# Kernel tuning notes

Hardware: AMD Instinct MI355X
Metric: run time of the kernel (lower is better)

## Reference

```python
import jax, jax.numpy as jnp
import numpy as np

NHEAD = 12
EPS = 1e-5


def layernorm_nobias(x, gamma):
    mu = jnp.mean(x, axis=-1, keepdims=True)
    var = jnp.var(x, axis=-1, keepdims=True)
    return (x - mu) * jax.lax.rsqrt(var + EPS) * gamma


def setup_inputs() -> dict:
    key = jax.random.key(0)
    ks = jax.random.split(key, 10)
    b, l, d = 4, 2048, 768
    s = d ** -0.5
    return {
        "x": jax.random.normal(ks[0], (b, l, d), jnp.float32),
        "Wq": jax.random.normal(ks[1], (d, d), jnp.float32) * s,
        "Wk": jax.random.normal(ks[2], (d, d), jnp.float32) * s,
        "bk": jax.random.normal(ks[3], (d,), jnp.float32) * 0.02,
        "Wv": jax.random.normal(ks[4], (d, d), jnp.float32) * s,
        "bv": jax.random.normal(ks[5], (d,), jnp.float32) * 0.02,
        "gq": jnp.ones((d,), jnp.float32),
        "gk": jnp.ones((d,), jnp.float32),
        "Wo": jax.random.normal(ks[6], (d, d), jnp.float32) * s,
        "bo": jnp.zeros((d,), jnp.float32),
    }


def reference(x, Wq, Wk, bk, Wv, bv, gq, gk, Wo, bo):
    b, l, d = x.shape
    n = NHEAD
    hd = d // n
    scale = hd ** -0.5
    # projections (torch Linear: x @ W.T + b), QK-norm over full dmodel
    q = layernorm_nobias(x @ Wq.T, gq)
    k = layernorm_nobias(x @ Wk.T + bk, gk)
    v = x @ Wv.T + bv
    # split heads: b l (n hd) -> b n l hd
    q = q.reshape(b, l, n, hd).transpose(0, 2, 1, 3)
    k = k.reshape(b, l, n, hd).transpose(0, 2, 1, 3)
    v = v.reshape(b, l, n, hd).transpose(0, 2, 1, 3)
    # scores [b, n, l_q, l_k]; NOTE: softmax over the QUERY axis (dim=-2)
    scores = jnp.einsum('bnqd,bnkd->bnqk', q, k) * scale
    attn = jax.nn.softmax(scores, axis=-2)
    o = jnp.einsum('bnqk,bnkd->bnqd', attn, v)
    o = o.transpose(0, 2, 1, 3).reshape(b, l, d)
    return o @ Wo.T + bo + x
```

## Files before the change

kernel.cpp:

```cpp
#include <hip/hip_runtime.h>
#include <cstddef>
#include <cstdint>


typedef unsigned short u16;
typedef short  bf16x8 __attribute__((ext_vector_type(8)));
typedef float  f32x4  __attribute__((ext_vector_type(4)));
typedef unsigned short u16x8 __attribute__((ext_vector_type(8)));
typedef unsigned short u16x4 __attribute__((ext_vector_type(4)));

#define B_   4
#define L_   2048
#define D_   768
#define NH_  12
#define HD_  64
#define M_   (B_*L_)
#define SC2  (0.125f * 1.44269504088896f)

__device__ __forceinline__ float ex2(float x) { return __builtin_amdgcn_exp2f(x); }

__device__ __forceinline__ u16 f2bf(float f) {
    union { float f; unsigned u; } v; v.f = f;
    unsigned r = v.u + 0x7FFFu + ((v.u >> 16) & 1u);
    return (u16)(r >> 16);
}
__device__ __forceinline__ float bf2f(u16 b) {
    union { unsigned u; float f; } v; v.u = ((unsigned)b) << 16;
    return v.f;
}
__device__ __forceinline__ unsigned fbits(float f) {
    union { float f; unsigned u; } v; v.f = f; return v.u;
}
__device__ __forceinline__ unsigned packbf(float lo, float hi) {
    return __builtin_amdgcn_perm(fbits(hi), fbits(lo), 0x07060302u);
}

__device__ __forceinline__ void gld16(const void* g, void* l) {
    __builtin_amdgcn_global_load_lds(
        (const __attribute__((address_space(1))) unsigned*)g,
        (__attribute__((address_space(3))) unsigned*)l, 16, 0, 0);
}

__global__ __launch_bounds__(256) void cvt_all(
    const float* __restrict__ X,
    const float* __restrict__ W0, const float* __restrict__ W1,
    const float* __restrict__ W2, const float* __restrict__ W3,
    u16* __restrict__ Yx,
    u16* __restrict__ Y0, u16* __restrict__ Y1,
    u16* __restrict__ Y2, u16* __restrict__ Y3)
{
    const int nX8 = (M_ * D_) / 8;
    const int nW8 = (D_ * D_) / 8;
    int i = blockIdx.x * 256 + threadIdx.x;
    if (i >= nX8 + 4 * nW8) return;
    const float* S; u16* Dst; int off;
    if (i < nX8) { S = X; Dst = Yx; off = i; }
    else {
        int j = i - nX8;
        int w = j / nW8; off = j - w * nW8;
        S   = (w == 0) ? W0 : (w == 1) ? W1 : (w == 2) ? W2 : W3;
        Dst = (w == 0) ? Y0 : (w == 1) ? Y1 : (w == 2) ? Y2 : Y3;
    }
    const float4* xp = (const float4*)S + (size_t)off * 2;
    float4 a = xp[0], b = xp[1];
    u16x8 o;
    o[0] = f2bf(a.x); o[1] = f2bf(a.y); o[2] = f2bf(a.z); o[3] = f2bf(a.w);
    o[4] = f2bf(b.x); o[5] = f2bf(b.y); o[6] = f2bf(b.z); o[7] = f2bf(b.w);
    *((u16x8*)Dst + off) = o;
}

__global__ __launch_bounds__(256, 4) void gemm_qkv(
    const u16* __restrict__ A,
    const u16* __restrict__ W0, const u16* __restrict__ W1,
    const u16* __restrict__ W2,
    const float* __restrict__ bk, const float* __restrict__ bv,
    u16* __restrict__ q_o, u16* __restrict__ k_o, u16* __restrict__ v_o)
{
    __shared__ __align__(16) u16 lds[16384];
    __shared__ float bs[128];
    const int tid  = threadIdx.x;
    const int lane = tid & 63, w = tid >> 6;
    const int s    = lane & 15, quad = lane >> 4;
    const int bid  = blockIdx.x;
    const int xcd  = bid & 7, j0 = bid >> 3;
    const int bm   = (xcd * 8 + j0 / 18) * 128;
    const int sub  = j0 % 18;
    const int seg  = sub / 6;
    const int bn   = (sub % 6) * 128;
    const u16* W = (seg == 0) ? W0 : ((seg == 1) ? W1 : W2);
    u16* OUT = (seg == 0) ? q_o : ((seg == 1) ? k_o : v_o);
    const int mh = (w >> 1) * 64, nh = (w & 1) * 64;
    const int wb = tid & ~63;
    const int cq = quad ^ ((s >> 1) & 3);

    if (tid < 128)
        bs[tid] = (seg == 1) ? bk[bn + tid] : ((seg == 2) ? bv[bn + tid] : 0.0f);

    f32x4 acc[4][4];
    #pragma unroll
    for (int j = 0; j < 4; ++j)
        #pragma unroll
        for (int i = 0; i < 4; ++i) acc[j][i] = (f32x4){0.f, 0.f, 0.f, 0.f};

    {
        int c = tid, r = c >> 2, cs = (c & 3) ^ ((r >> 1) & 3);
        gld16(A + (size_t)(bm + r) * D_ + cs * 8, lds + (size_t)wb * 8);
        gld16(W + (size_t)(bn + r) * D_ + cs * 8, lds + 8192 + (size_t)wb * 8);
        c = tid + 256; r = c >> 2; cs = (c & 3) ^ ((r >> 1) & 3);
        gld16(A + (size_t)(bm + r) * D_ + cs * 8, lds + (size_t)(wb + 256) * 8);
        gld16(W + (size_t)(bn + r) * D_ + cs * 8, lds + 8192 + (size_t)(wb + 256) * 8);
    }
    __syncthreads();

    for (int t = 0; t < 24; ++t) {
        const u16* Ab = lds + (t & 1) * 4096;
        const u16* Bb = lds + 8192 + (t & 1) * 4096;
        if (t < 23) {
            const int k0 = (t + 1) * 32;
            u16* Ad = lds + ((t + 1) & 1) * 4096;
            u16* Bd = lds + 8192 + ((t + 1) & 1) * 4096;
            int c = tid, r = c >> 2, cs = (c & 3) ^ ((r >> 1) & 3);
            gld16(A + (size_t)(bm + r) * D_ + k0 + cs * 8, Ad + (size_t)wb * 8);
            gld16(W + (size_t)(bn + r) * D_ + k0 + cs * 8, Bd + (size_t)wb * 8);
            c = tid + 256; r = c >> 2; cs = (c & 3) ^ ((r >> 1) & 3);
            gld16(A + (size_t)(bm + r) * D_ + k0 + cs * 8, Ad + (size_t)(wb + 256) * 8);
            gld16(W + (size_t)(bn + r) * D_ + k0 + cs * 8, Bd + (size_t)(wb + 256) * 8);
        }
        bf16x8 af[4], bf[4];
        #pragma unroll
        for (int i = 0; i < 4; ++i)
            af[i] = *(const bf16x8*)(Ab + (mh + i * 16 + s) * 32 + cq * 8);
        #pragma unroll
        for (int j = 0; j < 4; ++j)
            bf[j] = *(const bf16x8*)(Bb + (nh + j * 16 + s) * 32 + cq * 8);
        #pragma unroll
        for (int j = 0; j < 4; ++j)
            #pragma unroll
            for (int i = 0; i < 4; ++i)
                acc[j][i] = __builtin_amdgcn_mfma_f32_16x16x32_bf16(
                    bf[j], af[i], acc[j][i], 0, 0, 0);
        __syncthreads();
    }
    u16* Ct = lds;
    #pragma unroll
    for (int j = 0; j < 4; ++j) {
        const int n0 = nh + j * 16 + quad * 4;
        const f32x4 b4 = *(const f32x4*)(bs + n0);
        const int cn = n0 >> 3, off = n0 & 7;
        #pragma unroll
        for (int i = 0; i < 4; ++i) {
            const int m = mh + i * 16 + s;
            u16x4 ov;
            #pragma unroll
            for (int r = 0; r < 4; ++r) ov[r] = f2bf(acc[j][i][r] + b4[r]);
            *(u16x4*)(Ct + m * 128 + ((cn ^ (m & 15)) * 8) + off) = ov;
        }
    }
    __syncthreads();
    {
        const int m = tid >> 1, half = tid & 1;
        u16* dst = OUT + (size_t)(bm + m) * D_ + bn + half * 64;
        #pragma unroll
        for (int cc = 0; cc < 8; ++cc) {
            const int cn = half * 8 + cc;
            u16x8 v = *(const u16x8*)(Ct + m * 128 + ((cn ^ (m & 15)) * 8));
            *(u16x8*)(dst + cc * 8) = v;
        }
    }
}

__global__ __launch_bounds__(256, 3) void gemm_final(
    const u16* __restrict__ A, const u16* __restrict__ W,
    const float* __restrict__ bias, const float* __restrict__ resid,
    float* __restrict__ outf)
{
    __shared__ __align__(16) u16 lds[16384];
    const int tid  = threadIdx.x;
    const int lane = tid & 63, w = tid >> 6;
    const int s    = lane & 15, quad = lane >> 4;
    const int bid  = blockIdx.x;
    const int xcd  = bid & 7, j0 = bid >> 3;
    const int bm   = (xcd * 8 + j0 / 6) * 128;
    const int bn   = (j0 % 6) * 128;
    const int mh   = (w >> 1) * 64, nh = (w & 1) * 64;
    const int wb   = tid & ~63;
    const int cq   = quad ^ ((s >> 1) & 3);
    f32x4 acc[4][4];
    #pragma unroll
    for (int j = 0; j < 4; ++j)
        #pragma unroll
        for (int i = 0; i < 4; ++i) acc[j][i] = (f32x4){0.f, 0.f, 0.f, 0.f};

    {
        int c = tid, r = c >> 2, cs = (c & 3) ^ ((r >> 1) & 3);
        gld16(A + (size_t)(bm + r) * D_ + cs * 8, lds + (size_t)wb * 8);
        gld16(W + (size_t)(bn + r) * D_ + cs * 8, lds + 8192 + (size_t)wb * 8);
        c = tid + 256; r = c >> 2; cs = (c & 3) ^ ((r >> 1) & 3);
        gld16(A + (size_t)(bm + r) * D_ + cs * 8, lds + (size_t)(wb + 256) * 8);
        gld16(W + (size_t)(bn + r) * D_ + cs * 8, lds + 8192 + (size_t)(wb + 256) * 8);
    }
    __syncthreads();

    for (int t = 0; t < 24; ++t) {
        const u16* Ab = lds + (t & 1) * 4096;
        const u16* Bb = lds + 8192 + (t & 1) * 4096;
        if (t < 23) {
            const int k0 = (t + 1) * 32;
            u16* Ad = lds + ((t + 1) & 1) * 4096;
            u16* Bd = lds + 8192 + ((t + 1) & 1) * 4096;
            int c = tid, r = c >> 2, cs = (c & 3) ^ ((r >> 1) & 3);
            gld16(A + (size_t)(bm + r) * D_ + k0 + cs * 8, Ad + (size_t)wb * 8);
            gld16(W + (size_t)(bn + r) * D_ + k0 + cs * 8, Bd + (size_t)wb * 8);
            c = tid + 256; r = c >> 2; cs = (c & 3) ^ ((r >> 1) & 3);
            gld16(A + (size_t)(bm + r) * D_ + k0 + cs * 8, Ad + (size_t)(wb + 256) * 8);
            gld16(W + (size_t)(bn + r) * D_ + k0 + cs * 8, Bd + (size_t)(wb + 256) * 8);
        }
        bf16x8 af[4], bf[4];
        #pragma unroll
        for (int i = 0; i < 4; ++i)
            af[i] = *(const bf16x8*)(Ab + (mh + i * 16 + s) * 32 + cq * 8);
        #pragma unroll
        for (int j = 0; j < 4; ++j)
            bf[j] = *(const bf16x8*)(Bb + (nh + j * 16 + s) * 32 + cq * 8);
        #pragma unroll
        for (int j = 0; j < 4; ++j)
            #pragma unroll
            for (int i = 0; i < 4; ++i)
                acc[j][i] = __builtin_amdgcn_mfma_f32_16x16x32_bf16(
                    bf[j], af[i], acc[j][i], 0, 0, 0);
        __syncthreads();
    }
    #pragma unroll
    for (int j = 0; j < 4; ++j) {
        const int n0 = nh + j * 16 + quad * 4;
        const float4 b4 = *(const float4*)(bias + bn + n0);
        #pragma unroll
        for (int i = 0; i < 4; ++i) {
            const int m = mh + i * 16 + s;
            const size_t base = (size_t)(bm + m) * D_ + bn + n0;
            const float4 rs = *(const float4*)(resid + base);
            float4 o;
            o.x = acc[j][i][0] + b4.x + rs.x;
            o.y = acc[j][i][1] + b4.y + rs.y;
            o.z = acc[j][i][2] + b4.z + rs.z;
            o.w = acc[j][i][3] + b4.w + rs.w;
            *(float4*)(outf + base) = o;
        }
    }
}

__global__ __launch_bounds__(256) void ln2_bf16(
    const u16* __restrict__ Q, const u16* __restrict__ K,
    const float* __restrict__ gq, const float* __restrict__ gk,
    u16* __restrict__ Yq, u16* __restrict__ Yk)
{
    const int row = blockIdx.x;
    const int which = blockIdx.y;
    const u16* x = (which ? K : Q) + (size_t)row * D_;
    const float* gamma = which ? gk : gq;
    u16* Y = which ? Yk : Yq;
    const float scale = which ? 1.0f : (float)SC2;
    const int tid = threadIdx.x;
    float v[3];
    float lsum = 0.f, lsq = 0.f;
    #pragma unroll
    for (int e = 0; e < 3; ++e) {
        float t = bf2f(x[tid + e * 256]);
        v[e] = t; lsum += t; lsq += t * t;
    }
    #pragma unroll
    for (int off = 32; off > 0; off >>= 1) {
        lsum += __shfl_down(lsum, off);
        lsq  += __shfl_down(lsq,  off);
    }
    __shared__ float s1[4], s2[4];
    const int wv = tid >> 6, lane = tid & 63;
    if (lane == 0) { s1[wv] = lsum; s2[wv] = lsq; }
    __syncthreads();
    const float sum = s1[0] + s1[1] + s1[2] + s1[3];
    const float sq  = s2[0] + s2[1] + s2[2] + s2[3];
    const float mu  = sum * (1.0f / D_);
    const float var = sq * (1.0f / D_) - mu * mu;
    const float inv = rsqrtf(var + 1e-5f) * scale;
    #pragma unroll
    for (int e = 0; e < 3; ++e) {
        int c = tid + e * 256;
        Y[(size_t)row * D_ + c] = f2bf((v[e] - mu) * inv * gamma[c]);
    }
}

__global__ __launch_bounds__(256, 3) void attn_stats(
    const u16* __restrict__ Qb, const u16* __restrict__ Kb,
    float* __restrict__ Rl)
{
    __shared__ __align__(16) u16 Ks[128 * 64];
    __shared__ __align__(16) u16 Qs[2][128 * 64];
    __shared__ float lbuf[4][64];
    const int tid  = threadIdx.x;
    const int lane = tid & 63, w = tid >> 6;
    const int s    = lane & 15, quad = lane >> 4;
    const int s7   = s & 7;
    const int bid  = blockIdx.x;
    const int xcd  = bid & 7, j0 = bid >> 3;
    const int bh   = xcd * 6 + j0 / 16;
    const int kbase = (j0 % 16) * 128;
    const int b    = bh / NH_, h = bh % NH_;
    const u16* Qg = Qb + (size_t)b * L_ * D_ + h * HD_;
    const u16* Kg = Kb + (size_t)b * L_ * D_ + h * HD_;
    const int mh = (w >> 1) * 64;
    const int nh = (w & 1) * 64;
    const int wb = tid & ~63;

    #pragma unroll
    for (int c0 = 0; c0 < 1024; c0 += 256) {
        int c = c0 + tid, r = c >> 3, cc = (c & 7) ^ (r & 7);
        gld16(Kg + (size_t)(kbase + r) * D_ + cc * 8, Ks + (size_t)(c0 + wb) * 8);
        gld16(Qg + (size_t)r * D_ + cc * 8, Qs[0] + (size_t)(c0 + wb) * 8);
    }
    __syncthreads();
    bf16x8 kf[2][4];
    #pragma unroll
    for (int kk = 0; kk < 2; ++kk)
        #pragma unroll
        for (int i = 0; i < 4; ++i)
            kf[kk][i] = *(const bf16x8*)(Ks + (mh + i * 16 + s) * 64 +
                                         ((kk * 4 + quad) ^ s7) * 8);
    float lacc[4][4];
    #pragma unroll
    for (int i = 0; i < 4; ++i)
        #pragma unroll
        for (int r = 0; r < 4; ++r) lacc[i][r] = 0.f;

    for (int t = 0; t < 16; ++t) {
        if (t < 15) {
            const int qn = (t + 1) * 128;
            u16* Qd = Qs[(t + 1) & 1];
            #pragma unroll
            for (int c0 = 0; c0 < 1024; c0 += 256) {
                int c = c0 + tid, r = c >> 3, cc = (c & 7) ^ (r & 7);
                gld16(Qg + (size_t)(qn + r) * D_ + cc * 8, Qd + (size_t)(c0 + wb) * 8);
            }
        }
        const u16* Qt = Qs[t & 1];
        f32x4 acc[4][4];
        #pragma unroll
        for (int i = 0; i < 4; ++i)
            #pragma unroll
            for (int j = 0; j < 4; ++j) acc[i][j] = (f32x4){0.f, 0.f, 0.f, 0.f};
        #pragma unroll
        for (int kk = 0; kk < 2; ++kk) {
            bf16x8 bf[4];
            #pragma unroll
            for (int j = 0; j < 4; ++j)
                bf[j] = *(const bf16x8*)(Qt + (nh + j * 16 + s) * 64 +
                                         ((kk * 4 + quad) ^ s7) * 8);
            __builtin_amdgcn_s_setprio(1);
            #pragma unroll
            for (int i = 0; i < 4; ++i)
                #pragma unroll
                for (int j = 0; j < 4; ++j)
                    acc[i][j] = __builtin_amdgcn_mfma_f32_16x16x32_bf16(
                        kf[kk][i], bf[j], acc[i][j], 0, 0, 0);
            __builtin_amdgcn_s_setprio(0);
        }
        #pragma unroll
        for (int i = 0; i < 4; ++i)
            #pragma unroll
            for (int r = 0; r < 4; ++r) {
                float l0 = ex2(acc[i][0][r]) + ex2(acc[i][1][r]);
                float l1 = ex2(acc[i][2][r]) + ex2(acc[i][3][r]);
                lacc[i][r] += l0 + l1;
            }
        __syncthreads();
    }
    #pragma unroll
    for (int i = 0; i < 4; ++i)
        #pragma unroll
        for (int r = 0; r < 4; ++r) {
            float v = lacc[i][r];
            #pragma unroll
            for (int d2 = 1; d2 < 16; d2 <<= 1) v += __shfl_xor(v, d2);
            lacc[i][r] = v;
        }
    if (s == 0) {
        #pragma unroll
        for (int i = 0; i < 4; ++i)
            #pragma unroll
            for (int r = 0; r < 4; ++r)
                lbuf[w][i * 16 + quad * 4 + r] = lacc[i][r];
    }
    __syncthreads();
    if (tid < 128) {
        int kh = tid >> 6, kl = tid & 63;
        float l = lbuf[kh * 2][kl] + lbuf[kh * 2 + 1][kl];
        Rl[(size_t)bh * L_ + kbase + tid] = 1.0f / l;
    }
}

__global__ __launch_bounds__(256) void transpose_v_scaled(
    const u16* __restrict__ Vb, const float* __restrict__ Rl,
    u16* __restrict__ Vt)
{
    const int l0 = blockIdx.x * 64, h = blockIdx.y, b = blockIdx.z;
    const int bh = b * NH_ + h;
    __shared__ __align__(16) u16 Ts[64][72];
    const int tid = threadIdx.x;
    #pragma unroll
    for (int c = tid; c < 512; c += 256) {
        int r = c >> 3, cc = c & 7;
        u16x8 val = *(const u16x8*)(Vb + (size_t)(b * L_ + l0 + r) * D_ + h * HD_ + cc * 8);
        const float rl = Rl[(size_t)bh * L_ + l0 + r];
        #pragma unroll
        for (int e = 0; e < 8; ++e) val[e] = f2bf(bf2f(val[e]) * rl);
        *(u16x8*)(&Ts[r][cc * 8]) = val;
    }
    __syncthreads();
    const int d = tid >> 2, lc = (tid & 3) * 16;
    u16 tmp[16];
    #pragma unroll
    for (int e = 0; e < 16; ++e) tmp[e] = Ts[lc + e][d];
    u16* dst = Vt + ((size_t)bh * HD_ + d) * L_ + l0 + (lc & 32) + ((lc >> 4) & 1) * 4;
    #pragma unroll
    for (int qd = 0; qd < 4; ++qd) {
        u16x4 o;
        #pragma unroll
        for (int e = 0; e < 4; ++e) o[e] = tmp[qd * 4 + e];
        *(u16x4*)(dst + qd * 8) = o;
    }
}

__global__ __launch_bounds__(256, 3) void attn_out(
    const u16* __restrict__ Qb, const u16* __restrict__ Kb,
    const u16* __restrict__ Vt, u16* __restrict__ Ob)
{
    __shared__ __align__(16) u16 Ks[3][64 * 64];
    __shared__ __align__(16) u16 Vts[3][64 * 64];
    const int tid  = threadIdx.x;
    const int lane = tid & 63, w = tid >> 6;
    const int s    = lane & 15, quad = lane >> 4;
    const int s7   = s & 7;
    const int bid  = blockIdx.x;
    const int xcd  = bid & 7, j0 = bid >> 3;
    const int bh   = xcd * 6 + j0 / 16;
    const int qbase = (j0 % 16) * 128;
    const int b    = bh / NH_, h = bh % NH_;
    const int qw   = w * 32;
    const u16* Qg = Qb + (size_t)b * L_ * D_ + h * HD_;
    const u16* Kg = Kb + (size_t)b * L_ * D_ + h * HD_;
    const u16* Vg = Vt + (size_t)bh * HD_ * L_;
    const int wb = tid & ~63;

    bf16x8 qf[2][2];
    #pragma unroll
    for (int kk = 0; kk < 2; ++kk)
        #pragma unroll
        for (int j = 0; j < 2; ++j)
            qf[kk][j] = *(const bf16x8*)(
                Qg + (size_t)(qbase + qw + j * 16 + s) * D_ + (kk * 4 + quad) * 8);

    #pragma unroll
    for (int t0 = 0; t0 < 2; ++t0) {
        const int kn = t0 * 64;
        u16* Kd = Ks[t0];
        u16* Vd = Vts[t0];
        int c = tid, r = c >> 3, cc = (c & 7) ^ (r & 7);
        gld16(Kg + (size_t)(kn + r) * D_ + cc * 8, Kd + (size_t)wb * 8);
        gld16(Vg + (size_t)r * L_ + kn + cc * 8,   Vd + (size_t)wb * 8);
        c = tid + 256; r = c >> 3; cc = (c & 7) ^ (r & 7);
        gld16(Kg + (size_t)(kn + r) * D_ + cc * 8, Kd + (size_t)(wb + 256) * 8);
        gld16(Vg + (size_t)r * L_ + kn + cc * 8,   Vd + (size_t)(wb + 256) * 8);
    }
    __syncthreads();

    f32x4 acc_o[4][2];
    #pragma unroll
    for (int i = 0; i < 4; ++i)
        #pragma unroll
        for (int j = 0; j < 2; ++j) acc_o[i][j] = (f32x4){0.f, 0.f, 0.f, 0.f};

    for (int t = 0; t < 32; ++t) {
        const int bi = t % 3;
        const u16* Kt  = Ks[bi];
        const u16* Vtt = Vts[bi];
        if (t + 2 < 32) {
            const int pi = (t + 2) % 3;
            const int kn = (t + 2) * 64;
            u16* Kd = Ks[pi];
            u16* Vd = Vts[pi];
            int c = tid, r = c >> 3, cc = (c & 7) ^ (r & 7);
            gld16(Kg + (size_t)(kn + r) * D_ + cc * 8, Kd + (size_t)wb * 8);
            gld16(Vg + (size_t)r * L_ + kn + cc * 8,   Vd + (size_t)(wb) * 8);
            c = tid + 256; r = c >> 3; cc = (c & 7) ^ (r & 7);
            gld16(Kg + (size_t)(kn + r) * D_ + cc * 8, Kd + (size_t)(wb + 256) * 8);
            gld16(Vg + (size_t)r * L_ + kn + cc * 8,   Vd + (size_t)(wb + 256) * 8);
        }
        f32x4 acc_s[4][2];
        #pragma unroll
        for (int i = 0; i < 4; ++i)
            #pragma unroll
            for (int j = 0; j < 2; ++j) acc_s[i][j] = (f32x4){0.f, 0.f, 0.f, 0.f};
        #pragma unroll
        for (int kk = 0; kk < 2; ++kk) {
            bf16x8 kfr[4];
            #pragma unroll
            for (int i = 0; i < 4; ++i)
                kfr[i] = *(const bf16x8*)(Kt + (i * 16 + s) * 64 +
                                          ((kk * 4 + quad) ^ s7) * 8);
            __builtin_amdgcn_s_setprio(1);
            #pragma unroll
            for (int i = 0; i < 4; ++i)
                #pragma unroll
                for (int j = 0; j < 2; ++j)
                    acc_s[i][j] = __builtin_amdgcn_mfma_f32_16x16x32_bf16(
                        kfr[i], qf[kk][j], acc_s[i][j], 0, 0, 0);
            __builtin_amdgcn_s_setprio(0);
        }
        unsigned pk[4][2][2];
        #pragma unroll
        for (int i = 0; i < 4; ++i)
            #pragma unroll
            for (int j = 0; j < 2; ++j) {
                float p0 = ex2(acc_s[i][j][0]), p1 = ex2(acc_s[i][j][1]);
                float p2 = ex2(acc_s[i][j][2]), p3 = ex2(acc_s[i][j][3]);
                pk[i][j][0] = packbf(p0, p1);
                pk[i][j][1] = packbf(p2, p3);
            }
        #pragma unroll
        for (int kk = 0; kk < 2; ++kk) {
            bf16x8 av[4];
            #pragma unroll
            for (int i = 0; i < 4; ++i)
                av[i] = *(const bf16x8*)(Vtt + (i * 16 + s) * 64 +
                                         ((kk * 4 + quad) ^ s7) * 8);
            __builtin_amdgcn_s_setprio(1);
            #pragma unroll
            for (int j = 0; j < 2; ++j) {
                union { unsigned u[4]; bf16x8 v; } bu;
                bu.u[0] = pk[2 * kk][j][0];
                bu.u[1] = pk[2 * kk][j][1];
                bu.u[2] = pk[2 * kk + 1][j][0];
                bu.u[3] = pk[2 * kk + 1][j][1];
                #pragma unroll
                for (int i = 0; i < 4; ++i)
                    acc_o[i][j] = __builtin_amdgcn_mfma_f32_16x16x32_bf16(
                        av[i], bu.v, acc_o[i][j], 0, 0, 0);
            }
            __builtin_amdgcn_s_setprio(0);
        }
        if (t < 30) {
            asm volatile("s_waitcnt vmcnt(4)" ::: "memory");
            __builtin_amdgcn_s_barrier();
        } else if (t == 30) {
            asm volatile("s_waitcnt vmcnt(0)" ::: "memory");
            __builtin_amdgcn_s_barrier();
        }
    }
    __syncthreads();
    u16* Ep = (u16*)Ks;
    #pragma unroll
    for (int i = 0; i < 4; ++i) {
        const int dchunk = i * 2 + (quad >> 1), doff = (quad & 1) * 4;
        #pragma unroll
        for (int j = 0; j < 2; ++j) {
            const int q = qw + j * 16 + s;
            u16x4 ov;
            #pragma unroll
            for (int r = 0; r < 4; ++r) ov[r] = f2bf(acc_o[i][j][r]);
            *(u16x4*)(Ep + q * 64 + (dchunk ^ s7) * 8 + doff) = ov;
        }
    }
    __syncthreads();
    {
        const int q = tid >> 1, half = tid & 1, q7 = q & 7;
        u16* dst = Ob + (size_t)(b * L_ + qbase + q) * D_ + h * HD_ + half * 32;
        #pragma unroll
        for (int c = 0; c < 4; ++c) {
            const int cn = half * 4 + c;
            u16x8 v = *(const u16x8*)(Ep + q * 64 + ((cn ^ q7) * 8));
            *(u16x8*)(dst + c * 8) = v;
        }
    }
}

extern "C" void kernel_launch(void* const* d_in, const int* in_sizes, int n_in,
                              void* d_out, int out_size, void* d_ws, size_t ws_size,
                              hipStream_t stream)
{
    const float* x  = (const float*)d_in[0];
    const float* Wq = (const float*)d_in[1];
    const float* Wk = (const float*)d_in[2];
    const float* bk = (const float*)d_in[3];
    const float* Wv = (const float*)d_in[4];
    const float* bv = (const float*)d_in[5];
    const float* gq = (const float*)d_in[6];
    const float* gk = (const float*)d_in[7];
    const float* Wo = (const float*)d_in[8];
    const float* bo = (const float*)d_in[9];
    float* out = (float*)d_out;

    char* p = (char*)d_ws;
    u16* xb   = (u16*)p;  p += (size_t)M_ * D_ * 2;
    u16* qpre = (u16*)p;  p += (size_t)M_ * D_ * 2;
    u16* kpre = (u16*)p;  p += (size_t)M_ * D_ * 2;
    u16* vb   = (u16*)p;  p += (size_t)M_ * D_ * 2;
    u16* qb   = (u16*)p;  p += (size_t)M_ * D_ * 2;
    u16* kb   = (u16*)p;  p += (size_t)M_ * D_ * 2;
    u16* wqb  = (u16*)p;  p += (size_t)D_ * D_ * 2;
    u16* wkb  = (u16*)p;  p += (size_t)D_ * D_ * 2;
    u16* wvb  = (u16*)p;  p += (size_t)D_ * D_ * 2;
    u16* wob  = (u16*)p;  p += (size_t)D_ * D_ * 2;
    float* Rl = (float*)p; p += (size_t)B_ * NH_ * L_ * 4;
    u16* ob = qpre;
    u16* vt = kpre;

    const int nTot8 = (M_ * D_ + 4 * D_ * D_) / 8;
    cvt_all<<<(nTot8 + 255) / 256, 256, 0, stream>>>(
        x, Wq, Wk, Wv, Wo, xb, wqb, wkb, wvb, wob);

    gemm_qkv<<<1152, 256, 0, stream>>>(
        xb, wqb, wkb, wvb, bk, bv, qpre, kpre, vb);

    ln2_bf16<<<dim3(M_, 2), 256, 0, stream>>>(qpre, kpre, gq, gk, qb, kb);

    attn_stats<<<768, 256, 0, stream>>>(qb, kb, Rl);
    transpose_v_scaled<<<dim3(L_ / 64, NH_, B_), 256, 0, stream>>>(vb, Rl, vt);
    attn_out<<<768, 256, 0, stream>>>(qb, kb, vt, ob);

    gemm_final<<<384, 256, 0, stream>>>(ob, wob, bo, x, out);
}
```

Baseline: 273.6 us.

## Software-pipeline attention loop so next tile's QK^T overlaps current tile's PV

Restructures the attention inner loop into a two-stage software pipeline. The scores for tile t+1 are computed with MFMA while tile t's exp2 and PV MFMAs run, using two ping-pong score accumulators. The loop is unrolled by two via a macro. The prologue is also reordered to issue K loads before V loads and to wait only for K(0..1) and V0 (vmcnt(2)) rather than a full sync, so the first QK^T starts earlier. The aim is to hide the exp/pack latency and the dependency stall between QK^T and PV, at the cost of more accumulator registers, which may reduce occupancy. The priority boost on the QK MFMAs is dropped.

```diff
diff --git a/kernel.cpp b/kernel.cpp
--- a/kernel.cpp
+++ b/kernel.cpp
@@ -458,19 +458,20 @@
             qf[kk][j] = *(const bf16x8*)(
                 Qg + (size_t)(qbase + qw + j * 16 + s) * D_ + (kk * 4 + quad) * 8);
 
-    #pragma unroll
-    for (int t0 = 0; t0 < 2; ++t0) {
-        const int kn = t0 * 64;
-        u16* Kd = Ks[t0];
-        u16* Vd = Vts[t0];
+    {
         int c = tid, r = c >> 3, cc = (c & 7) ^ (r & 7);
-        gld16(Kg + (size_t)(kn + r) * D_ + cc * 8, Kd + (size_t)wb * 8);
-        gld16(Vg + (size_t)r * L_ + kn + cc * 8,   Vd + (size_t)wb * 8);
-        c = tid + 256; r = c >> 3; cc = (c & 7) ^ (r & 7);
-        gld16(Kg + (size_t)(kn + r) * D_ + cc * 8, Kd + (size_t)(wb + 256) * 8);
-        gld16(Vg + (size_t)r * L_ + kn + cc * 8,   Vd + (size_t)(wb + 256) * 8);
-    }
-    __syncthreads();
+        int c2 = tid + 256, r2 = c2 >> 3, cc2 = (c2 & 7) ^ (r2 & 7);
+        gld16(Kg + (size_t)r * D_ + cc * 8,          Ks[0] + (size_t)wb * 8);
+        gld16(Kg + (size_t)r2 * D_ + cc2 * 8,        Ks[0] + (size_t)(wb + 256) * 8);
+        gld16(Kg + (size_t)(64 + r) * D_ + cc * 8,   Ks[1] + (size_t)wb * 8);
+        gld16(Kg + (size_t)(64 + r2) * D_ + cc2 * 8, Ks[1] + (size_t)(wb + 256) * 8);
+        gld16(Vg + (size_t)r * L_ + cc * 8,          Vts[0] + (size_t)wb * 8);
+        gld16(Vg + (size_t)r2 * L_ + cc2 * 8,        Vts[0] + (size_t)(wb + 256) * 8);
+        gld16(Vg + (size_t)r * L_ + 64 + cc * 8,     Vts[1] + (size_t)wb * 8);
+        gld16(Vg + (size_t)r2 * L_ + 64 + cc2 * 8,   Vts[1] + (size_t)(wb + 256) * 8);
+    }
+    asm volatile("s_waitcnt vmcnt(2)" ::: "memory");
+    __builtin_amdgcn_s_barrier();
 
     f32x4 acc_o[4][2];
     #pragma unroll
@@ -478,83 +479,120 @@
         #pragma unroll
         for (int j = 0; j < 2; ++j) acc_o[i][j] = (f32x4){0.f, 0.f, 0.f, 0.f};
 
-    for (int t = 0; t < 32; ++t) {
-        const int bi = t % 3;
-        const u16* Kt  = Ks[bi];
-        const u16* Vtt = Vts[bi];
-        if (t + 2 < 32) {
-            const int pi = (t + 2) % 3;
-            const int kn = (t + 2) * 64;
-            u16* Kd = Ks[pi];
-            u16* Vd = Vts[pi];
-            int c = tid, r = c >> 3, cc = (c & 7) ^ (r & 7);
-            gld16(Kg + (size_t)(kn + r) * D_ + cc * 8, Kd + (size_t)wb * 8);
-            gld16(Vg + (size_t)r * L_ + kn + cc * 8,   Vd + (size_t)(wb) * 8);
-            c = tid + 256; r = c >> 3; cc = (c & 7) ^ (r & 7);
-            gld16(Kg + (size_t)(kn + r) * D_ + cc * 8, Kd + (size_t)(wb + 256) * 8);
-            gld16(Vg + (size_t)r * L_ + kn + cc * 8,   Vd + (size_t)(wb + 256) * 8);
-        }
-        f32x4 acc_s[4][2];
-        #pragma unroll
-        for (int i = 0; i < 4; ++i)
-            #pragma unroll
-            for (int j = 0; j < 2; ++j) acc_s[i][j] = (f32x4){0.f, 0.f, 0.f, 0.f};
-        #pragma unroll
-        for (int kk = 0; kk < 2; ++kk) {
-            bf16x8 kfr[4];
-            #pragma unroll
-            for (int i = 0; i < 4; ++i)
-                kfr[i] = *(const bf16x8*)(Kt + (i * 16 + s) * 64 +
-                                          ((kk * 4 + quad) ^ s7) * 8);
-            __builtin_amdgcn_s_setprio(1);
-            #pragma unroll
-            for (int i = 0; i < 4; ++i)
-                #pragma unroll
-                for (int j = 0; j < 2; ++j)
-                    acc_s[i][j] = __builtin_amdgcn_mfma_f32_16x16x32_bf16(
-                        kfr[i], qf[kk][j], acc_s[i][j], 0, 0, 0);
-            __builtin_amdgcn_s_setprio(0);
-        }
-        unsigned pk[4][2][2];
-        #pragma unroll
-        for (int i = 0; i < 4; ++i)
-            #pragma unroll
-            for (int j = 0; j < 2; ++j) {
-                float p0 = ex2(acc_s[i][j][0]), p1 = ex2(acc_s[i][j][1]);
-                float p2 = ex2(acc_s[i][j][2]), p3 = ex2(acc_s[i][j][3]);
-                pk[i][j][0] = packbf(p0, p1);
-                pk[i][j][1] = packbf(p2, p3);
-            }
-        #pragma unroll
-        for (int kk = 0; kk < 2; ++kk) {
-            bf16x8 av[4];
-            #pragma unroll
-            for (int i = 0; i < 4; ++i)
-                av[i] = *(const bf16x8*)(Vtt + (i * 16 + s) * 64 +
-                                         ((kk * 4 + quad) ^ s7) * 8);
-            __builtin_amdgcn_s_setprio(1);
-            #pragma unroll
-            for (int j = 0; j < 2; ++j) {
-                union { unsigned u[4]; bf16x8 v; } bu;
-                bu.u[0] = pk[2 * kk][j][0];
-                bu.u[1] = pk[2 * kk][j][1];
-                bu.u[2] = pk[2 * kk + 1][j][0];
-                bu.u[3] = pk[2 * kk + 1][j][1];
-                #pragma unroll
-                for (int i = 0; i < 4; ++i)
-                    acc_o[i][j] = __builtin_amdgcn_mfma_f32_16x16x32_bf16(
-                        av[i], bu.v, acc_o[i][j], 0, 0, 0);
-            }
-            __builtin_amdgcn_s_setprio(0);
-        }
-        if (t < 30) {
-            asm volatile("s_waitcnt vmcnt(4)" ::: "memory");
-            __builtin_amdgcn_s_barrier();
-        } else if (t == 30) {
-            asm volatile("s_waitcnt vmcnt(0)" ::: "memory");
-            __builtin_amdgcn_s_barrier();
-        }
-    }
+    f32x4 acc_s0[4][2], acc_s1[4][2];
+    #pragma unroll
+    for (int i = 0; i < 4; ++i)
+        #pragma unroll
+        for (int j = 0; j < 2; ++j) acc_s0[i][j] = (f32x4){0.f, 0.f, 0.f, 0.f};
+    #pragma unroll
+    for (int kk = 0; kk < 2; ++kk) {
+        bf16x8 kfr[4];
+        #pragma unroll
+        for (int i = 0; i < 4; ++i)
+            kfr[i] = *(const bf16x8*)(Ks[0] + (i * 16 + s) * 64 +
+                                      ((kk * 4 + quad) ^ s7) * 8);
+        #pragma unroll
+        for (int i = 0; i < 4; ++i)
+            #pragma unroll
+            for (int j = 0; j < 2; ++j)
+                acc_s0[i][j] = __builtin_amdgcn_mfma_f32_16x16x32_bf16(
+                    kfr[i], qf[kk][j], acc_s0[i][j], 0, 0, 0);
+    }
+
+#define ATTN_TILE(ACCC, ACCN, TT, DO_PF, DO_S, WMODE)                          \
+    do {                                                                       \
+        const int t_ = (TT);                                                   \
+        if (DO_PF) {                                                           \
+            const int pi_ = (t_ + 2) % 3;                                      \
+            const int kn_ = (t_ + 2) * 64;                                     \
+            u16* Kd_ = Ks[pi_]; u16* Vd_ = Vts[pi_];                           \
+            int c_ = tid, r_ = c_ >> 3, cc_ = (c_ & 7) ^ (r_ & 7);             \
+            int c2_ = tid + 256, r2_ = c2_ >> 3, cc2_ = (c2_ & 7) ^ (r2_ & 7); \
+            gld16(Kg + (size_t)(kn_ + r_) * D_ + cc_ * 8,                      \
+                  Kd_ + (size_t)wb * 8);                                       \
+            gld16(Kg + (size_t)(kn_ + r2_) * D_ + cc2_ * 8,                    \
+                  Kd_ + (size_t)(wb + 256) * 8);                               \
+            gld16(Vg + (size_t)r_ * L_ + kn_ + cc_ * 8,                        \
+                  Vd_ + (size_t)wb * 8);                                       \
+            gld16(Vg + (size_t)r2_ * L_ + kn_ + cc2_ * 8,                      \
+                  Vd_ + (size_t)(wb + 256) * 8);                               \
+        }                                                                      \
+                 \
+        unsigned pk_[4][2][2];                                                 \
+        _Pragma("unroll")                                                      \
+        for (int i = 0; i < 4; ++i)                                            \
+            _Pragma("unroll")                                                  \
+            for (int j = 0; j < 2; ++j) {                                      \
+                float p0_ = ex2(ACCC[i][j][0]), p1_ = ex2(ACCC[i][j][1]);      \
+                float p2_ = ex2(ACCC[i][j][2]), p3_ = ex2(ACCC[i][j][3]);      \
+                pk_[i][j][0] = packbf(p0_, p1_);                               \
+                pk_[i][j][1] = packbf(p2_, p3_);                               \
+            }                                                                  \
+        if (DO_S) {                                                            \
+            const u16* Kt_ = Ks[(t_ + 1) % 3];                                 \
+            _Pragma("unroll")                                                  \
+            for (int i = 0; i < 4; ++i)                                        \
+                _Pragma("unroll")                                              \
+                for (int j = 0; j < 2; ++j)                                    \
+                    ACCN[i][j] = (f32x4){0.f, 0.f, 0.f, 0.f};                  \
+            _Pragma("unroll")                                                  \
+            for (int kk = 0; kk < 2; ++kk) {                                   \
+                bf16x8 kfr_[4];                                                \
+                _Pragma("unroll")                                              \
+                for (int i = 0; i < 4; ++i)                                    \
+                    kfr_[i] = *(const bf16x8*)(Kt_ + (i * 16 + s) * 64 +       \
+                                               ((kk * 4 + quad) ^ s7) * 8);    \
+                _Pragma("unroll")                                              \
+                for (int i = 0; i < 4; ++i)                                    \
+                    _Pragma("unroll")                                          \
+                    for (int j = 0; j < 2; ++j)                                \
+                        ACCN[i][j] = __builtin_amdgcn_mfma_f32_16x16x32_bf16(  \
+                            kfr_[i], qf[kk][j], ACCN[i][j], 0, 0, 0);          \
+            }                                                                  \
+        }                                                                      \
+                                                                   \
+        {                                                                      \
+            const u16* Vtt_ = Vts[t_ % 3];                                     \
+            _Pragma("unroll")                                                  \
+            for (int kk = 0; kk < 2; ++kk) {                                   \
+                bf16x8 av_[4];                                                 \
+                _Pragma("unroll")                                              \
+                for (int i = 0; i < 4; ++i)                                    \
+                    av_[i] = *(const bf16x8*)(Vtt_ + (i * 16 + s) * 64 +       \
+                                              ((kk * 4 + quad) ^ s7) * 8);     \
+                __builtin_amdgcn_s_setprio(1);                                 \
+                _Pragma("unroll")                                              \
+                for (int j = 0; j < 2; ++j) {                                  \
+                    union { unsigned u[4]; bf16x8 v; } bu_;                    \
+                    bu_.u[0] = pk_[2 * kk][j][0];                              \
+                    bu_.u[1] = pk_[2 * kk][j][1];                              \
+                    bu_.u[2] = pk_[2 * kk + 1][j][0];                          \
+                    bu_.u[3] = pk_[2 * kk + 1][j][1];                          \
+                    _Pragma("unroll")                                          \
+                    for (int i = 0; i < 4; ++i)                                \
+                        acc_o[i][j] = __builtin_amdgcn_mfma_f32_16x16x32_bf16( \
+                            av_[i], bu_.v, acc_o[i][j], 0, 0, 0);              \
+                }                                                              \
+                __builtin_amdgcn_s_setprio(0);                                 \
+            }                                                                  \
+        }                                                                      \
+        if (WMODE == 2) {                                                      \
+            asm volatile("s_waitcnt vmcnt(2)" ::: "memory");                   \
+            __builtin_amdgcn_s_barrier();                                      \
+        } else if (WMODE == 0) {                                               \
+            asm volatile("s_waitcnt vmcnt(0)" ::: "memory");                   \
+            __builtin_amdgcn_s_barrier();                                      \
+        }                                                                      \
+    } while (0)
+
+    for (int t = 0; t < 30; t += 2) {
+        ATTN_TILE(acc_s0, acc_s1, t,     1, 1, 2);
+        ATTN_TILE(acc_s1, acc_s0, t + 1, 1, 1, 2);
+    }
+    ATTN_TILE(acc_s0, acc_s1, 30, 0, 1, 0);
+    ATTN_TILE(acc_s1, acc_s0, 31, 0, 0, -1);
+#undef ATTN_TILE
+
     __syncthreads();
     u16* Ep = (u16*)Ks;
     #pragma unroll
```

Result: no change. 276.3 us (+1.0%).
